# Kernel optimization log

Measured on AMD Instinct MI355X. Metric: run time of the kernel, lower is better.

## Reference

```python
import jax, jax.numpy as jnp
import numpy as np

B, S, I, Q, H = 512, 196, 2048, 1024, 512


def _attn(X, g, wx, bx, wg, bg, wh, bh):
    # X: (B, S, F); g: (B, G) or None
    feat = jnp.einsum('bsf,fh->bsh', X, wx) + bx
    if g is not None:
        feat = feat + (g @ wg + bg)[:, None, :]
    h = jnp.tanh(feat)
    score = jnp.einsum('bsh,h->bs', h, wh) + bh  # (B, S)
    a = jax.nn.softmax(score, axis=1)
    return jnp.einsum('bs,bsf->bf', a, X)


def setup_inputs() -> dict:
    key = jax.random.key(0)
    ks = jax.random.split(key, 16)
    sc = lambda n: 1.0 / np.sqrt(n)
    d = {
        'ques_feat': jax.random.normal(ks[0], (B, Q), jnp.float32),
        'img_feat': jax.random.normal(ks[1], (B, S, I), jnp.float32),
        # attn1: X=ques (Q), no guidance
        'w1x': jax.random.uniform(ks[2], (Q, H), jnp.float32, -sc(Q), sc(Q)),
        'b1x': jnp.zeros((H,), jnp.float32),
        'w1h': jax.random.uniform(ks[3], (H,), jnp.float32, -sc(H), sc(H)),
        'b1h': jnp.zeros((), jnp.float32),
        # attn2: X=img (I), guidance=ques (Q)
        'w2x': jax.random.uniform(ks[4], (I, H), jnp.float32, -sc(I), sc(I)),
        'b2x': jnp.zeros((H,), jnp.float32),
        'w2g': jax.random.uniform(ks[5], (Q, H), jnp.float32, -sc(Q), sc(Q)),
        'b2g': jnp.zeros((H,), jnp.float32),
        'w2h': jax.random.uniform(ks[6], (H,), jnp.float32, -sc(H), sc(H)),
        'b2h': jnp.zeros((), jnp.float32),
        # attn3: X=ques (Q), guidance=img-attended (I)
        'w3x': jax.random.uniform(ks[7], (Q, H), jnp.float32, -sc(Q), sc(Q)),
        'b3x': jnp.zeros((H,), jnp.float32),
        'w3g': jax.random.uniform(ks[8], (I, H), jnp.float32, -sc(I), sc(I)),
        'b3g': jnp.zeros((H,), jnp.float32),
        'w3h': jax.random.uniform(ks[9], (H,), jnp.float32, -sc(H), sc(H)),
        'b3h': jnp.zeros((), jnp.float32),
    }
    return d


def reference(ques_feat, img_feat, w1x, b1x, w1h, b1h, w2x, b2x, w2g, b2g,
              w2h, b2h, w3x, b3x, w3g, b3g, w3h, b3h):
    q = ques_feat[:, None, :]  # (B, 1, Q)
    ques_self = _attn(q, None, w1x, b1x, None, None, w1h, b1h)          # (B, Q)
    img_attn = _attn(img_feat, ques_self, w2x, b2x, w2g, b2g, w2h, b2h)  # (B, I)
    ques_attn = _attn(q, img_attn, w3x, b3x, w3g, b3g, w3h, b3h)         # (B, Q)
    return (ques_attn, img_attn)
```

## Files before the change

kernel.cpp:

```cpp
#include <hip/hip_runtime.h>
#include <hip/hip_bf16.h>
#include <cstdint>


typedef __attribute__((ext_vector_type(8))) short bf16x8;
typedef __attribute__((ext_vector_type(4))) float f32x4;

typedef __attribute__((address_space(1))) const unsigned int as1_uint;
typedef __attribute__((address_space(3))) unsigned int as3_uint;

__device__ inline unsigned short f2bf(float f) {
    union { float f; unsigned u; } v; v.f = f;
    unsigned u = v.u;
    u += 0x7FFFu + ((u >> 16) & 1u);
    return (unsigned short)(u >> 16);
}

__device__ inline unsigned pk2(float lo, float hi) {
    __hip_bfloat162 h = __float22bfloat162_rn(make_float2(lo, hi));
    return *reinterpret_cast<unsigned*>(&h);
}

__device__ inline unsigned pkq(unsigned a, unsigned b) {
    union { unsigned u; float f; } x, y; x.u = a; y.u = b;
    return pk2(x.f, y.f);
}

__device__ inline bf16x8 cvt8(uint4 lo, uint4 hi) {
    union { unsigned u[4]; bf16x8 v; } r;
    r.u[0] = pkq(lo.x, lo.y); r.u[1] = pkq(lo.z, lo.w);
    r.u[2] = pkq(hi.x, hi.y); r.u[3] = pkq(hi.z, hi.w);
    return r.v;
}

__global__ void k_pack_w(const float* __restrict__ w, unsigned short* __restrict__ wtf) {
    int kblk = blockIdx.x >> 5;
    int nblk = blockIdx.x & 31;
    int t = threadIdx.x;
    int kc8 = t >> 4, col = t & 15;
    const float* src = w + (size_t)(kblk * 64 + kc8 * 8) * 512 + nblk * 16 + col;
    unsigned short* dst = wtf + (size_t)(kblk * 32 + nblk) * 1024 + kc8 * 128 + col * 8;
    unsigned short tmp[8];
    #pragma unroll
    for (int j = 0; j < 8; ++j) tmp[j] = f2bf(src[(size_t)j * 512]);
    *reinterpret_cast<uint4*>(dst) = *reinterpret_cast<const uint4*>(tmp);
}

__global__ void k_cconst(const float* __restrict__ qf, const float* __restrict__ w2g,
                         const float* __restrict__ b2g, const float* __restrict__ b2x,
                         float* __restrict__ cc, float* __restrict__ out0) {
    __shared__ float qls[2][1024];
    int b0 = blockIdx.x * 2;
    int t = threadIdx.x;
    #pragma unroll
    for (int j = 0; j < 2; ++j) {
        int idx = j * 256 + t;
        int bb = idx >> 8, c4 = idx & 255;
        float4 v = reinterpret_cast<const float4*>(qf + (size_t)(b0 + bb) * 1024)[c4];
        qls[bb][c4 * 4 + 0] = v.x; qls[bb][c4 * 4 + 1] = v.y;
        qls[bb][c4 * 4 + 2] = v.z; qls[bb][c4 * 4 + 3] = v.w;
        reinterpret_cast<float4*>(out0 + (size_t)(b0 + bb) * 1024)[c4] = v;
    }
    __syncthreads();
    float a00 = 0.f, a01 = 0.f, a10 = 0.f, a11 = 0.f;
    #pragma unroll 8
    for (int q = 0; q < 1024; ++q) {
        float w0 = w2g[q * 512 + t];
        float w1 = w2g[q * 512 + 256 + t];
        float q0 = qls[0][q], q1 = qls[1][q];
        a00 += q0 * w0; a01 += q0 * w1;
        a10 += q1 * w0; a11 += q1 * w1;
    }
    float c0 = b2g[t] + b2x[t];
    float c1 = b2g[t + 256] + b2x[t + 256];
    cc[(size_t)b0 * 512 + t] = a00 + c0;
    cc[(size_t)b0 * 512 + t + 256] = a01 + c1;
    cc[(size_t)(b0 + 1) * 512 + t] = a10 + c0;
    cc[(size_t)(b0 + 1) * 512 + t + 256] = a11 + c1;
}

#define NSTEP 32

__global__ __launch_bounds__(512, 4) void k_scores(
    const float* __restrict__ X, const unsigned short* __restrict__ WTf,
    const float* __restrict__ cc, const float* __restrict__ w2h,
    float* __restrict__ scores)
{
    __shared__ __align__(16) char Ab[4][16384];
    __shared__ float slds[64];

    int tid = threadIdx.x;
    int wave = tid >> 6, lane = tid & 63;
    int l15 = lane & 15, l4 = lane >> 4;
    int r0 = blockIdx.x * 64;

    int srow = tid >> 4, spc = tid & 15;
    const char* xsrc = reinterpret_cast<const char*>(X + (size_t)(r0 + srow) * 2048)
                       + ((spc ^ (srow & 15)) << 4);
    const char* xsrc2 = xsrc + (size_t)32 * 8192;
    char* ldsw = &Ab[0][0] + wave * 1024;

    const unsigned short* wb0 = WTf + (size_t)wave * 4096 + l4 * 128 + l15 * 8;

    const char* abase = &Ab[0][0];
    int off00 = l15 * 256 + (((l4 * 2 + 0) ^ l15) << 4);
    int off01 = l15 * 256 + (((l4 * 2 + 1) ^ l15) << 4);
    int off10 = l15 * 256 + (((8 + l4 * 2 + 0) ^ l15) << 4);
    int off11 = l15 * 256 + (((8 + l4 * 2 + 1) ^ l15) << 4);

    if (tid < 64) slds[tid] = 0.0f;

    f32x4 acc[4][4];
    #pragma unroll
    for (int m = 0; m < 4; ++m)
        #pragma unroll
        for (int n = 0; n < 4; ++n) acc[m][n] = (f32x4){0.f, 0.f, 0.f, 0.f};

    bf16x8 brA[4], brB[4];

    #define GLOAD2(bufofs, step) do { \
        __builtin_amdgcn_global_load_lds((as1_uint*)(xsrc + (step) * 256), \
            (as3_uint*)(ldsw + (bufofs)), 16, 0, 2); \
        __builtin_amdgcn_global_load_lds((as1_uint*)(xsrc2 + (step) * 256), \
            (as3_uint*)(ldsw + (bufofs) + 8192), 16, 0, 2); } while (0)

    #define BLOAD(dst, t, kh) do { \
        const unsigned short* bp = wb0 + (size_t)(t) * 32768 + (kh) * 512; \
        dst[0] = *reinterpret_cast<const bf16x8*>(bp); \
        dst[1] = *reinterpret_cast<const bf16x8*>(bp + 1024); \
        dst[2] = *reinterpret_cast<const bf16x8*>(bp + 2048); \
        dst[3] = *reinterpret_cast<const bf16x8*>(bp + 3072); } while (0)

    #define MF(br, bufofs, offL, offH) do { \
        __builtin_amdgcn_s_setprio(1); \
        _Pragma("unroll") \
        for (int m = 0; m < 4; ++m) { \
            uint4 lo = *reinterpret_cast<const uint4*>(abase + (bufofs) + m * 4096 + (offL)); \
            uint4 hi = *reinterpret_cast<const uint4*>(abase + (bufofs) + m * 4096 + (offH)); \
            bf16x8 af = cvt8(lo, hi); \
            _Pragma("unroll") \
            for (int n = 0; n < 4; ++n) \
                acc[m][n] = __builtin_amdgcn_mfma_f32_16x16x32_bf16(af, br[n], acc[m][n], 0, 0, 0); \
        } \
        __builtin_amdgcn_s_setprio(0); } while (0)

    #define SBAR __builtin_amdgcn_sched_barrier(0)

    GLOAD2(0, 0);
    GLOAD2(16384, 1);
    GLOAD2(32768, 2);
    BLOAD(brA, 0, 0);
    asm volatile("s_waitcnt vmcnt(8)" ::: "memory");
    __builtin_amdgcn_s_barrier();

    #pragma unroll 1
    for (int t = 0; t < NSTEP; ++t) {
        int bufofs = (t & 3) * 16384;
        BLOAD(brB, t, 1);
        MF(brA, bufofs, off00, off01);
        if (t + 1 < NSTEP) BLOAD(brA, t + 1, 0);
        MF(brB, bufofs, off10, off11);
        SBAR;
        if (t + 3 < NSTEP) GLOAD2(((t + 3) & 3) * 16384, t + 3);
        SBAR;
        __builtin_amdgcn_s_barrier();
    }

    asm volatile("" ::: "memory");

    int b0 = r0 / 196;
    int sbreak = (b0 + 1) * 196 - r0;
    int b1 = b0 + 1; if (b1 > 511) b1 = 511;
    float cch0[4], cch1[4], whv[4];
    #pragma unroll
    for (int n = 0; n < 4; ++n) {
        int h = wave * 64 + n * 16 + l15;
        cch0[n] = cc[(size_t)b0 * 512 + h];
        cch1[n] = cc[(size_t)b1 * 512 + h];
        whv[n] = w2h[h];
    }
    #pragma unroll
    for (int m = 0; m < 4; ++m) {
        #pragma unroll
        for (int i = 0; i < 4; ++i) {
            int row = m * 16 + l4 * 4 + i;
            float p = 0.0f;
            #pragma unroll
            for (int n = 0; n < 4; ++n) {
                float x = acc[m][n][i] + ((row < sbreak) ? cch0[n] : cch1[n]);
                float th = 1.0f - 2.0f / (__expf(2.0f * x) + 1.0f);
                p += th * whv[n];
            }
            p += __shfl_xor(p, 1);
            p += __shfl_xor(p, 2);
            p += __shfl_xor(p, 4);
            p += __shfl_xor(p, 8);
            if (l15 == 0) atomicAdd(&slds[row], p);
        }
    }
    __syncthreads();
    if (tid < 64) scores[(size_t)r0 + tid] = slds[tid];
}

__global__ __launch_bounds__(256) void k_wsum_sm(const float* __restrict__ X,
                                                 const float* __restrict__ sc,
                                                 float* __restrict__ out1) {
    __shared__ float als[196];
    __shared__ float red[8];
    int b = blockIdx.x >> 1;
    int fh = (blockIdx.x & 1) * 1024;
    int t = threadIdx.x;

    float v = (t < 196) ? sc[(size_t)b * 196 + t] : -3.0e38f;
    float m = v;
    for (int o = 32; o > 0; o >>= 1) m = fmaxf(m, __shfl_xor(m, o));
    if ((t & 63) == 0) red[t >> 6] = m;
    __syncthreads();
    m = fmaxf(fmaxf(red[0], red[1]), fmaxf(red[2], red[3]));
    float e = (t < 196) ? __expf(v - m) : 0.0f;
    float s = e;
    for (int o = 32; o > 0; o >>= 1) s += __shfl_xor(s, o);
    if ((t & 63) == 0) red[4 + (t >> 6)] = s;
    __syncthreads();
    float tot = red[4] + red[5] + red[6] + red[7];
    if (t < 196) als[t] = e / tot;
    __syncthreads();

    int f = fh + t * 4;
    const float* Xb = X + (size_t)b * 196 * 2048 + f;
    float4 acc = {0.f, 0.f, 0.f, 0.f};
    #pragma unroll 4
    for (int ss = 0; ss < 196; ++ss) {
        float4 x = *reinterpret_cast<const float4*>(Xb + (size_t)ss * 2048);
        float w = als[ss];
        acc.x += w * x.x; acc.y += w * x.y; acc.z += w * x.z; acc.w += w * x.w;
    }
    *reinterpret_cast<float4*>(out1 + (size_t)b * 2048 + f) = acc;
}

extern "C" void kernel_launch(void* const* d_in, const int* in_sizes, int n_in,
                              void* d_out, int out_size, void* d_ws, size_t ws_size,
                              hipStream_t stream) {
    const float* qf  = (const float*)d_in[0];
    const float* X   = (const float*)d_in[1];
    const float* w2x = (const float*)d_in[6];
    const float* b2x = (const float*)d_in[7];
    const float* w2g = (const float*)d_in[8];
    const float* b2g = (const float*)d_in[9];
    const float* w2h = (const float*)d_in[10];

    float* out0 = (float*)d_out;
    float* out1 = out0 + 512 * 1024;

    unsigned short* WTf = (unsigned short*)d_ws;
    float* cc = (float*)((char*)d_ws + (size_t)(2u << 20));
    float* sc = (float*)((char*)d_ws + (size_t)(3u << 20));

    k_pack_w<<<1024, 128, 0, stream>>>(w2x, WTf);
    k_cconst<<<256, 256, 0, stream>>>(qf, w2g, b2g, b2x, cc, out0);
    k_scores<<<1568, 512, 0, stream>>>(X, WTf, cc, w2h, sc);
    k_wsum_sm<<<1024, 256, 0, stream>>>(X, sc, out1);
}
```

Before: 523.9 us.

## Convert fp32 A tile to bf16 once per block into a double-buffered LDS tile

Previously each of the eight waves read the fp32 X tile from LDS and converted it to bf16 on its own, repeating the same reads and conversions eight times. Now all threads cooperatively convert the next step's fp32 tile once into a swizzled, double-buffered bf16 LDS region. The MFMA loop then reads ready-made bf16 fragments with a single 16-byte load per m. This is meant to cut LDS read traffic and VALU conversion work, at the cost of an extra 16 KB of LDS (which may affect occupancy) and an added lgkmcnt wait before each barrier.

```diff
diff --git a/kernel.cpp b/kernel.cpp
--- a/kernel.cpp
+++ b/kernel.cpp
@@ -87,6 +87,7 @@
     float* __restrict__ scores)
 {
     __shared__ __align__(16) char Ab[4][16384];
+    __shared__ __align__(16) char Bb[2][8192];
     __shared__ float slds[64];
 
     int tid = threadIdx.x;
@@ -100,13 +101,17 @@
     const char* xsrc2 = xsrc + (size_t)32 * 8192;
     char* ldsw = &Ab[0][0] + wave * 1024;
 
+    int cr = tid >> 3, co = tid & 7;
+    int cvt_fL = cr * 256 + (((2 * co) ^ (cr & 15)) << 4);
+    int cvt_fH = cr * 256 + (((2 * co + 1) ^ (cr & 15)) << 4);
+    int cvt_w  = cr * 128 + ((co ^ (cr & 7)) << 4);
+
     const unsigned short* wb0 = WTf + (size_t)wave * 4096 + l4 * 128 + l15 * 8;
 
     const char* abase = &Ab[0][0];
-    int off00 = l15 * 256 + (((l4 * 2 + 0) ^ l15) << 4);
-    int off01 = l15 * 256 + (((l4 * 2 + 1) ^ l15) << 4);
-    int off10 = l15 * 256 + (((8 + l4 * 2 + 0) ^ l15) << 4);
-    int off11 = l15 * 256 + (((8 + l4 * 2 + 1) ^ l15) << 4);
+    char* bbase = &Bb[0][0];
+    int voffK0 = l15 * 128 + ((l4 ^ (l15 & 7)) << 4);
+    int voffK1 = l15 * 128 + (((4 + l4) ^ (l15 & 7)) << 4);
 
     if (tid < 64) slds[tid] = 0.0f;
 
@@ -131,13 +136,16 @@
         dst[2] = *reinterpret_cast<const bf16x8*>(bp + 2048); \
         dst[3] = *reinterpret_cast<const bf16x8*>(bp + 3072); } while (0)
 
-    #define MF(br, bufofs, offL, offH) do { \
+    #define CONVERT(fbo, bbo) do { \
+        uint4 lo = *reinterpret_cast<const uint4*>(abase + (fbo) + cvt_fL); \
+        uint4 hi = *reinterpret_cast<const uint4*>(abase + (fbo) + cvt_fH); \
+        *reinterpret_cast<bf16x8*>(bbase + (bbo) + cvt_w) = cvt8(lo, hi); } while (0)
+
+    #define MF(br, bbo, voffK) do { \
         __builtin_amdgcn_s_setprio(1); \
         _Pragma("unroll") \
         for (int m = 0; m < 4; ++m) { \
-            uint4 lo = *reinterpret_cast<const uint4*>(abase + (bufofs) + m * 4096 + (offL)); \
-            uint4 hi = *reinterpret_cast<const uint4*>(abase + (bufofs) + m * 4096 + (offH)); \
-            bf16x8 af = cvt8(lo, hi); \
+            bf16x8 af = *reinterpret_cast<const bf16x8*>(bbase + (bbo) + m * 2048 + (voffK)); \
             _Pragma("unroll") \
             for (int n = 0; n < 4; ++n) \
                 acc[m][n] = __builtin_amdgcn_mfma_f32_16x16x32_bf16(af, br[n], acc[m][n], 0, 0, 0); \
@@ -151,18 +159,22 @@
     GLOAD2(32768, 2);
     BLOAD(brA, 0, 0);
     asm volatile("s_waitcnt vmcnt(8)" ::: "memory");
+    CONVERT(0, 0);
+    asm volatile("s_waitcnt lgkmcnt(0)" ::: "memory");
     __builtin_amdgcn_s_barrier();
 
     #pragma unroll 1
     for (int t = 0; t < NSTEP; ++t) {
-        int bufofs = (t & 3) * 16384;
+        int bbo = (t & 1) * 8192;
         BLOAD(brB, t, 1);
-        MF(brA, bufofs, off00, off01);
+        MF(brA, bbo, voffK0);
         if (t + 1 < NSTEP) BLOAD(brA, t + 1, 0);
-        MF(brB, bufofs, off10, off11);
+        MF(brB, bbo, voffK1);
+        if (t + 1 < NSTEP) CONVERT(((t + 1) & 3) * 16384, ((t + 1) & 1) * 8192);
         SBAR;
         if (t + 3 < NSTEP) GLOAD2(((t + 3) & 3) * 16384, t + 3);
         SBAR;
+        asm volatile("s_waitcnt lgkmcnt(0)" ::: "memory");
         __builtin_amdgcn_s_barrier();
     }
 
```

New measurement: 592.4 us. 13.1% more time.
